# Performance work log

Measured on AMD Instinct MI355X. Metric: run time of the kernel, lower is better.

## Reference

```python
import jax, jax.numpy as jnp
import numpy as np

N, E, D, R, G, C = 100000, 600000, 128, 4, 256, 16
EPS = 1e-5

def _rgcn(x, src, dst, edge_type, w_rel, w_root, b):
    # out_i = x_i @ W_root + b + sum_r mean_{j in N_r(i)} x_j @ W_r  (PyG RGCNConv, aggr='mean')
    x_src = x[src]                                   # [E, D] gather
    out = x @ w_root + b                             # [N, D]
    for r in range(R):
        m = (edge_type == r).astype(x.dtype)         # [E]
        msg = (x_src @ w_rel[r]) * m[:, None]        # [E, D]
        agg = jax.ops.segment_sum(msg, dst, num_segments=N)
        cnt = jax.ops.segment_sum(m, dst, num_segments=N)
        out = out + agg / jnp.maximum(cnt, 1.0)[:, None]
    return out

def _bn_eval(x, gamma, beta, mean, var):
    return (x - mean) * jax.lax.rsqrt(var + EPS) * gamma + beta

def setup_inputs() -> dict:
    key = jax.random.key(0)
    ks = jax.random.split(key, 12)
    x = jax.random.normal(ks[0], (N, D), dtype=jnp.float32)
    edge_index = jax.random.randint(ks[1], (2, E), 0, N)
    edge_type = jax.random.randint(ks[2], (E,), 0, R)
    batch = jnp.sort(jax.random.randint(ks[3], (N,), 0, G))
    s = 1.0 / np.sqrt(D)
    conv_rel_w = jax.random.normal(ks[4], (3, R, D, D), dtype=jnp.float32) * s
    conv_root_w = jax.random.normal(ks[5], (3, D, D), dtype=jnp.float32) * s
    conv_bias = jnp.zeros((3, D), dtype=jnp.float32)
    bn_gamma = jnp.ones((2, D), dtype=jnp.float32)
    bn_beta = jnp.zeros((2, D), dtype=jnp.float32)
    bn_mean = jax.random.normal(ks[6], (2, D), dtype=jnp.float32) * 0.1
    bn_var = jax.random.uniform(ks[7], (2, D), minval=0.5, maxval=1.5, dtype=jnp.float32)
    cls_w1 = jax.random.normal(ks[8], (D, D // 2), dtype=jnp.float32) * s
    cls_b1 = jnp.zeros((D // 2,), dtype=jnp.float32)
    cls_w2 = jax.random.normal(ks[9], (D // 2, C), dtype=jnp.float32) / np.sqrt(D // 2)
    cls_b2 = jnp.zeros((C,), dtype=jnp.float32)
    return {"x": x, "edge_index": edge_index, "edge_type": edge_type, "batch": batch,
            "conv_rel_w": conv_rel_w, "conv_root_w": conv_root_w, "conv_bias": conv_bias,
            "bn_gamma": bn_gamma, "bn_beta": bn_beta, "bn_mean": bn_mean, "bn_var": bn_var,
            "cls_w1": cls_w1, "cls_b1": cls_b1, "cls_w2": cls_w2, "cls_b2": cls_b2}

def reference(x, edge_index, edge_type, batch, conv_rel_w, conv_root_w, conv_bias,
              bn_gamma, bn_beta, bn_mean, bn_var, cls_w1, cls_b1, cls_w2, cls_b2):
    src, dst = edge_index[0], edge_index[1]
    prev = None
    h = x
    for i in range(3):
        h_new = _rgcn(h, src, dst, edge_type, conv_rel_w[i], conv_root_w[i], conv_bias[i])
        if prev is not None:
            h_new = h_new + prev  # residual (shapes always match: D==D)
        if i != 2:
            h_new = _bn_eval(h_new, bn_gamma[i], bn_beta[i], bn_mean[i], bn_var[i])
            h_new = jax.nn.elu(h_new)  # alpha=1; dropout inactive in eval
        prev = h_new
        h = h_new
    # global mean pool over graphs
    sums = jax.ops.segment_sum(h, batch, num_segments=G)          # [G, D]
    cnts = jax.ops.segment_sum(jnp.ones((N,), h.dtype), batch, num_segments=G)
    pooled = sums / jnp.maximum(cnts, 1.0)[:, None]
    z = jax.nn.elu(pooled @ cls_w1 + cls_b1)
    logits = z @ cls_w2 + cls_b2
    return jax.nn.log_softmax(logits, axis=-1)
```

## Files before the change

kernel.cpp:

```cpp
#include <hip/hip_runtime.h>
#include <hip/hip_bf16.h>

#define NN 100000
#define EE 600000
#define DD 128
#define GG 256
#define CCL 16

typedef __attribute__((ext_vector_type(8))) short short8;
typedef __attribute__((ext_vector_type(4))) float f32x4;
typedef const __attribute__((address_space(1))) void* gas_t;
typedef __attribute__((address_space(3))) void* las_t;

__device__ __forceinline__ void async_ld16(const void* g, void* l) {
    __builtin_amdgcn_global_load_lds((gas_t)g, (las_t)l, 16, 0, 0);
}
__device__ __forceinline__ unsigned short f2bf(float x) {
    unsigned u = __float_as_uint(x);
    unsigned r = (u + 0x7FFFu + ((u >> 16) & 1u)) >> 16;
    return (unsigned short)r;
}
__device__ __forceinline__ float bf2f(unsigned short b) {
    return __uint_as_float(((unsigned)b) << 16);
}
__device__ __forceinline__ void unpack8(uint4 v, float* f) {
    f[0] = __uint_as_float(v.x << 16); f[1] = __uint_as_float(v.x & 0xFFFF0000u);
    f[2] = __uint_as_float(v.y << 16); f[3] = __uint_as_float(v.y & 0xFFFF0000u);
    f[4] = __uint_as_float(v.z << 16); f[5] = __uint_as_float(v.z & 0xFFFF0000u);
    f[6] = __uint_as_float(v.w << 16); f[7] = __uint_as_float(v.w & 0xFFFF0000u);
}

__global__ __launch_bounds__(256) void sniff_kernel(const void* __restrict__ xraw, int* __restrict__ flag) {
    int t = threadIdx.x;
    const unsigned short* u = (const unsigned short*)xraw;
    int good = 0;
    #pragma unroll
    for (int i = 0; i < 4; i++) {
        unsigned short b = u[t * 4 + i];
        int e = (b >> 7) & 0xFF;
        if (e >= 107 && e <= 130) good++;
    }
    __shared__ int sg[256];
    sg[t] = good;
    __syncthreads();
    for (int s = 128; s > 0; s >>= 1) { if (t < s) sg[t] += sg[t + s]; __syncthreads(); }
    if (t == 0) flag[0] = (sg[0] >= 900) ? 1 : 0;
}

__device__ __forceinline__ float loadf(const void* p, size_t i, int isbf) {
    if (isbf) return bf2f(((const unsigned short*)p)[i]);
    return ((const float*)p)[i];
}

__global__ __launch_bounds__(256) void convx_kernel(const void* __restrict__ xraw, const int* __restrict__ flag,
                                                    __hip_bfloat16* __restrict__ xc) {
    int isbf = flag[0];
    size_t i0 = ((size_t)blockIdx.x * 256 + threadIdx.x) * 8;
    if (i0 >= (size_t)NN * DD) return;
    if (isbf) {
        *(uint4*)(xc + i0) = *(const uint4*)((const __hip_bfloat16*)xraw + i0);
    } else {
        const float* xf = (const float*)xraw;
        unsigned short o[8];
        #pragma unroll
        for (int j = 0; j < 8; j++) o[j] = f2bf(xf[i0 + j]);
        *(uint4*)(xc + i0) = *(uint4*)o;
    }
}

__global__ __launch_bounds__(256) void convw_kernel(const void* __restrict__ rel_raw, const void* __restrict__ root_raw,
                                                    const int* __restrict__ flag, __hip_bfloat16* __restrict__ wt) {
    int isbf = flag[0];
    int mat = blockIdx.x;
    int layer = mat / 5, g = mat % 5;
    size_t srcoff = (g == 0) ? (size_t)layer * 16384 : (size_t)(layer * 4 + (g - 1)) * 16384;
    const void* sraw = (g == 0) ? root_raw : rel_raw;
    __hip_bfloat16* dstp = wt + (size_t)mat * 16384;
    for (int idx = threadIdx.x; idx < 16384; idx += 256) {
        int k = idx >> 7, n = idx & 127;
        float v = loadf(sraw, srcoff + (size_t)k * 128 + n, isbf);
        dstp[n * 128 + k] = __float2bfloat16(v);
    }
}

__global__ __launch_bounds__(256) void convp_kernel(const void* bias, const void* bng, const void* bnb,
                                                    const void* bnm, const void* bnv, const void* w1,
                                                    const void* b1, const void* w2, const void* b2,
                                                    const int* __restrict__ flag, float* __restrict__ pf) {
    int isbf = flag[0];
    const void* srcs[9] = {bias, bng, bnb, bnm, bnv, w1, b1, w2, b2};
    const int cnts[9] = {384, 256, 256, 256, 256, 8192, 64, 1024, 16};
    const int offs[9] = {0, 384, 640, 896, 1152, 1408, 9600, 9664, 10688};
    int b = blockIdx.x;
    const void* s = srcs[b];
    int c = cnts[b], o = offs[b];
    for (int i = threadIdx.x; i < c; i += 256) pf[o + i] = loadf(s, i, isbf);
}

__global__ __launch_bounds__(256) void count_kernel(const int* __restrict__ dst, int* __restrict__ cnt) {
    int e = blockIdx.x * 256 + threadIdx.x;
    if (e < EE) atomicAdd(&cnt[dst[e]], 1);
}

__global__ __launch_bounds__(256) void alloc_kernel(const int* __restrict__ cnt, int* __restrict__ counter,
                                                    int* __restrict__ startp, int* __restrict__ wptr) {
    int n = blockIdx.x * 256 + threadIdx.x;
    int lane = threadIdx.x & 63;
    int c = (n < NN) ? cnt[n] : 0;
    int v = c;
    #pragma unroll
    for (int d = 1; d < 64; d <<= 1) {
        int o = __shfl_up(v, d);
        if (lane >= d) v += o;
    }
    int base = 0;
    if (lane == 63) base = atomicAdd(counter, v);
    base = __shfl(base, 63);
    if (n < NN) {
        int s = base + v - c;
        startp[n] = s;
        wptr[n]  = s;
    }
}

__global__ __launch_bounds__(256) void fill_kernel(const int* __restrict__ src, const int* __restrict__ dst,
                                                   const int* __restrict__ et, int* __restrict__ wptr,
                                                   int* __restrict__ elist) {
    int e = blockIdx.x * 256 + threadIdx.x;
    if (e < EE) {
        int d = dst[e];
        int pos = atomicAdd(&wptr[d], 1);
        elist[pos] = src[e] | (et[e] << 17);
    }
}

__global__ __launch_bounds__(256) void agg_kernel(const __hip_bfloat16* __restrict__ h,
                                                  const int* __restrict__ elist,
                                                  const int* __restrict__ startp,
                                                  const int* __restrict__ cnt,
                                                  __hip_bfloat16* __restrict__ xagg) {
    int wid = (blockIdx.x * 256 + threadIdx.x) >> 6;
    int lane = threadIdx.x & 63;
    if (wid >= NN) return;
    int s = startp[wid], c = cnt[wid];
    int egrp = lane >> 4, col16 = lane & 15;
    int my = (lane < c) ? elist[s + lane] : 0;
    float acc[4][8];
    float cc[4] = {0.f, 0.f, 0.f, 0.f};
    #pragma unroll
    for (int rr = 0; rr < 4; rr++)
        #pragma unroll
        for (int j = 0; j < 8; j++) acc[rr][j] = 0.f;

    for (int base = 0; base < c; base += 8) {
        int eA = base + egrp, eB = base + 4 + egrp;
        bool actA = eA < c, actB = eB < c;
        int pA = __shfl(my, eA & 63);
        int pB = __shfl(my, eB & 63);
        if (actA && eA >= 64) pA = elist[s + eA];
        if (actB && eB >= 64) pB = elist[s + eB];
        int srcA = pA & 0x1FFFF, rA = (pA >> 17) & 3;
        int srcB = pB & 0x1FFFF, rB = (pB >> 17) & 3;
        uint4 vA = make_uint4(0, 0, 0, 0), vB = make_uint4(0, 0, 0, 0);
        if (actA) vA = *(const uint4*)(h + (size_t)srcA * DD + col16 * 8);
        if (actB) vB = *(const uint4*)(h + (size_t)srcB * DD + col16 * 8);
        float fA[8], fB[8];
        unpack8(vA, fA);
        unpack8(vB, fB);
        #pragma unroll
        for (int rr = 0; rr < 4; rr++) {
            float mA = (actA && rA == rr) ? 1.f : 0.f;
            float mB = (actB && rB == rr) ? 1.f : 0.f;
            cc[rr] += mA + mB;
            #pragma unroll
            for (int j = 0; j < 8; j++)
                acc[rr][j] = fmaf(mA, fA[j], fmaf(mB, fB[j], acc[rr][j]));
        }
    }
    #pragma unroll
    for (int rr = 0; rr < 4; rr++) {
        cc[rr] += __shfl_xor(cc[rr], 16);
        cc[rr] += __shfl_xor(cc[rr], 32);
        #pragma unroll
        for (int j = 0; j < 8; j++) {
            float sv = acc[rr][j];
            sv += __shfl_xor(sv, 16);
            sv += __shfl_xor(sv, 32);
            acc[rr][j] = sv;
        }
    }
    float o[8], ct;
    #pragma unroll
    for (int j = 0; j < 8; j++)
        o[j] = egrp < 2 ? (egrp == 0 ? acc[0][j] : acc[1][j])
                        : (egrp == 2 ? acc[2][j] : acc[3][j]);
    ct = egrp < 2 ? (egrp == 0 ? cc[0] : cc[1]) : (egrp == 2 ? cc[2] : cc[3]);
    float inv = 1.f / fmaxf(ct, 1.f);
    unsigned short u[8];
    #pragma unroll
    for (int j = 0; j < 8; j++) u[j] = f2bf(o[j] * inv);
    *(uint4*)(xagg + (size_t)wid * 512 + egrp * 128 + col16 * 8) = *(uint4*)u;
}

__global__ __launch_bounds__(256, 4) void gemm_kernel(const __hip_bfloat16* __restrict__ h_in,
                                                      const __hip_bfloat16* __restrict__ xagg,
                                                      const __hip_bfloat16* __restrict__ wt,
                                                      const float* __restrict__ bias,
                                                      const float* __restrict__ bng,
                                                      const float* __restrict__ bnb,
                                                      const float* __restrict__ bnm,
                                                      const float* __restrict__ bnv,
                                                      const __hip_bfloat16* __restrict__ hres,
                                                      __hip_bfloat16* __restrict__ hout,
                                                      int do_bn) {
    __shared__ __align__(16) short lds[16384];
    __shared__ float sbias[128], sgm[128], sga[128];
    short* Ab = lds;
    short* Bb = lds + 8192;
    int t = threadIdx.x;
    int wave = t >> 6, lane = t & 63, quad = lane >> 4, r16 = lane & 15;
    int m0 = blockIdx.x * 128;

    if (t < 128) {
        sbias[t] = bias[t];
        float gm = 0.f, ga = 0.f;
        if (do_bn) {
            float iva = rsqrtf(bnv[t] + 1e-5f);
            gm = bng[t] * iva;
            ga = bnb[t] - bnm[t] * gm;
        }
        sgm[t] = gm; sga[t] = ga;
    }

    int rbase = t >> 3;
    int gseg8 = ((t & 7) ^ (rbase & 7)) * 8;

    f32x4 acc[2][8];
    #pragma unroll
    for (int i = 0; i < 2; i++)
        #pragma unroll
        for (int j = 0; j < 8; j++) acc[i][j] = (f32x4){0.f, 0.f, 0.f, 0.f};

    for (int c = 0; c < 10; c++) {
        const __hip_bfloat16* asrc;
        int astride;
        if (c < 2) { asrc = h_in + c * 64; astride = 128; }
        else       { asrc = xagg + (c - 2) * 64; astride = 512; }
        const __hip_bfloat16* bsrc = wt + (size_t)(c >> 1) * 16384 + (c & 1) * 64;
        #pragma unroll
        for (int j = 0; j < 4; j++) {
            int row = j * 32 + rbase;
            int node = m0 + row; if (node > NN - 1) node = NN - 1;
            async_ld16(asrc + (size_t)node * astride + gseg8, &Ab[(j * 256 + t) * 8]);
            async_ld16(bsrc + (size_t)row * 128 + gseg8, &Bb[(j * 256 + t) * 8]);
        }
        __syncthreads();
        #pragma unroll
        for (int kc = 0; kc < 2; kc++) {
            int ra0 = wave * 32 + r16;
            int ra1 = ra0 + 16;
            short8 a0 = *(const short8*)&Ab[(ra0 * 8 + ((kc * 4 + quad) ^ (ra0 & 7))) * 8];
            short8 a1 = *(const short8*)&Ab[(ra1 * 8 + ((kc * 4 + quad) ^ (ra1 & 7))) * 8];
            #pragma unroll
            for (int nt = 0; nt < 8; nt++) {
                int rb = nt * 16 + r16;
                short8 b = *(const short8*)&Bb[(rb * 8 + ((kc * 4 + quad) ^ (rb & 7))) * 8];
                acc[0][nt] = __builtin_amdgcn_mfma_f32_16x16x32_bf16(a0, b, acc[0][nt], 0, 0, 0);
                acc[1][nt] = __builtin_amdgcn_mfma_f32_16x16x32_bf16(a1, b, acc[1][nt], 0, 0, 0);
            }
        }
        __syncthreads();
    }

    #pragma unroll
    for (int nt = 0; nt < 8; nt++) {
        int col = nt * 16 + r16;
        float bv = sbias[col];
        #pragma unroll
        for (int mt = 0; mt < 2; mt++) {
            #pragma unroll
            for (int reg = 0; reg < 4; reg++) {
                int row = wave * 32 + mt * 16 + quad * 4 + reg;
                int sslot = (col >> 3) ^ (row & 15);
                lds[row * 128 + sslot * 8 + (col & 7)] = (short)f2bf(acc[mt][nt][reg] + bv);
            }
        }
    }
    __syncthreads();
    int row = t >> 1, half = t & 1;
    int node = m0 + row;
    if (node < NN) {
        #pragma unroll
        for (int q = 0; q < 8; q++) {
            int seg = half * 8 + q;
            int sslot = seg ^ (row & 15);
            short8 cv = *(const short8*)&lds[row * 128 + sslot * 8];
            int col0 = seg * 8;
            float v[8];
            #pragma unroll
            for (int j = 0; j < 8; j++) v[j] = bf2f((unsigned short)cv[j]);
            if (hres) {
                float rf[8];
                unpack8(*(const uint4*)(hres + (size_t)node * 128 + col0), rf);
                #pragma unroll
                for (int j = 0; j < 8; j++) v[j] += rf[j];
            }
            if (do_bn) {
                #pragma unroll
                for (int j = 0; j < 8; j++) {
                    float z = v[j] * sgm[col0 + j] + sga[col0 + j];
                    v[j] = z > 0.f ? z : expm1f(z);
                }
            }
            unsigned short u[8];
            #pragma unroll
            for (int j = 0; j < 8; j++) u[j] = f2bf(v[j]);
            *(uint4*)(hout + (size_t)node * 128 + col0) = *(uint4*)u;
        }
    }
}

__global__ __launch_bounds__(256) void pool_kernel(const __hip_bfloat16* __restrict__ h3,
                                                   const int* __restrict__ batch,
                                                   float* __restrict__ pooled) {
    int g = blockIdx.x, t = threadIdx.x;
    int rowpar = t >> 4, colg = t & 15;
    int lo = 0, hi = NN;
    while (lo < hi) { int mid = (lo + hi) >> 1; if (batch[mid] < g) lo = mid + 1; else hi = mid; }
    int s0 = lo;
    hi = NN;
    while (lo < hi) { int mid = (lo + hi) >> 1; if (batch[mid] < g + 1) lo = mid + 1; else hi = mid; }
    int s1 = lo;
    float a[8];
    #pragma unroll
    for (int j = 0; j < 8; j++) a[j] = 0.f;
    for (int n = s0 + rowpar; n < s1; n += 16) {
        float f[8];
        unpack8(*(const uint4*)(h3 + (size_t)n * 128 + colg * 8), f);
        #pragma unroll
        for (int j = 0; j < 8; j++) a[j] += f[j];
    }
    __shared__ float sd[16][128];
    #pragma unroll
    for (int j = 0; j < 8; j++) sd[rowpar][colg * 8 + j] = a[j];
    __syncthreads();
    if (t < 128) {
        float sum = 0.f;
        #pragma unroll
        for (int i = 0; i < 16; i++) sum += sd[i][t];
        int cgn = s1 - s0;
        pooled[g * 128 + t] = sum / (float)(cgn > 0 ? cgn : 1);
    }
}

__global__ __launch_bounds__(64) void cls_kernel(const float* __restrict__ pooled,
                                                 const float* __restrict__ pf,
                                                 const int* __restrict__ flag,
                                                 void* __restrict__ out) {
    int g = blockIdx.x, j = threadIdx.x;
    const float* w1 = pf + 1408;
    const float* b1 = pf + 9600;
    const float* w2 = pf + 9664;
    const float* b2 = pf + 10688;
    __shared__ float z[64];
    __shared__ float lg[16];
    const float* p = pooled + g * 128;
    float acc = b1[j];
    for (int d = 0; d < 128; d++) acc += p[d] * w1[d * 64 + j];
    acc = acc > 0.f ? acc : expm1f(acc);
    z[j] = acc;
    __syncthreads();
    if (j < CCL) {
        float l = b2[j];
        for (int k = 0; k < 64; k++) l += z[k] * w2[k * 16 + j];
        lg[j] = l;
    }
    __syncthreads();
    if (j < CCL) {
        float m = lg[0];
        for (int k = 1; k < CCL; k++) m = fmaxf(m, lg[k]);
        float s = 0.f;
        for (int k = 0; k < CCL; k++) s += expf(lg[k] - m);
        float val = lg[j] - m - logf(s);
        if (flag[0]) ((__hip_bfloat16*)out)[g * CCL + j] = __float2bfloat16(val);
        else         ((float*)out)[g * CCL + j] = val;
    }
}

extern "C" void kernel_launch(void* const* d_in, const int* in_sizes, int n_in,
                              void* d_out, int out_size, void* d_ws, size_t ws_size,
                              hipStream_t stream) {
    const void* x_raw    = d_in[0];
    const int* ei        = (const int*)d_in[1];
    const int* et        = (const int*)d_in[2];
    const int* batch     = (const int*)d_in[3];
    const void* rel_raw  = d_in[4];
    const void* root_raw = d_in[5];
    const int* srcp = ei;
    const int* dstp = ei + EE;

    char* ws = (char*)d_ws;
    size_t off = 0;
    auto take = [&](size_t bytes) { size_t r = off; off += (bytes + 1023) & ~(size_t)1023; return r; };
    __hip_bfloat16* xagg = (__hip_bfloat16*)(ws + take((size_t)NN * 512 * 2));
    __hip_bfloat16* xc   = (__hip_bfloat16*)(ws + take((size_t)NN * 128 * 2));
    __hip_bfloat16* hA   = (__hip_bfloat16*)(ws + take((size_t)NN * 128 * 2));
    __hip_bfloat16* hB   = (__hip_bfloat16*)(ws + take((size_t)NN * 128 * 2));
    __hip_bfloat16* hC   = (__hip_bfloat16*)(ws + take((size_t)NN * 128 * 2));
    __hip_bfloat16* wt   = (__hip_bfloat16*)(ws + take((size_t)15 * 16384 * 2));
    float* pf            = (float*)(ws + take((size_t)10704 * 4));
    float* pooled        = (float*)(ws + take((size_t)GG * 128 * 4));
    int* cnt             = (int*)(ws + take((size_t)NN * 4 + 8));
    int* counter         = cnt + NN;
    int* flag            = cnt + NN + 1;
    int* startp          = (int*)(ws + take((size_t)NN * 4));
    int* wptr            = (int*)(ws + take((size_t)NN * 4));
    int* elist           = (int*)(ws + take((size_t)EE * 4));

    hipMemsetAsync(cnt, 0, (size_t)NN * 4 + 4, stream);
    sniff_kernel<<<1, 256, 0, stream>>>(x_raw, flag);
    convx_kernel<<<(NN * DD / 8 + 255) / 256, 256, 0, stream>>>(x_raw, flag, xc);
    convw_kernel<<<15, 256, 0, stream>>>(rel_raw, root_raw, flag, wt);
    convp_kernel<<<9, 256, 0, stream>>>(d_in[6], d_in[7], d_in[8], d_in[9], d_in[10],
                                        d_in[11], d_in[12], d_in[13], d_in[14], flag, pf);
    count_kernel<<<(EE + 255) / 256, 256, 0, stream>>>(dstp, cnt);
    alloc_kernel<<<(NN + 255) / 256, 256, 0, stream>>>(cnt, counter, startp, wptr);
    fill_kernel<<<(EE + 255) / 256, 256, 0, stream>>>(srcp, dstp, et, wptr, elist);

    const __hip_bfloat16* hin = xc;
    __hip_bfloat16* houts[3] = {hA, hB, hC};
    for (int l = 0; l < 3; l++) {
        agg_kernel<<<(NN * 64 + 255) / 256, 256, 0, stream>>>(hin, elist, startp, cnt, xagg);
        int bl = l < 2 ? l : 1;
        gemm_kernel<<<(NN + 127) / 128, 256, 0, stream>>>(
            hin, xagg, wt + (size_t)l * 5 * 16384, pf + l * 128,
            pf + 384 + bl * 128, pf + 640 + bl * 128, pf + 896 + bl * 128, pf + 1152 + bl * 128,
            (l > 0) ? hin : (const __hip_bfloat16*)nullptr, houts[l], (l < 2) ? 1 : 0);
        hin = houts[l];
    }
    pool_kernel<<<GG, 256, 0, stream>>>(houts[2], batch, pooled);
    cls_kernel<<<GG, 64, 0, stream>>>(pooled, pf, flag, (void*)d_out);
}
```

Measured before the change: 700.6 us.

## Bucket edges by (dst, relation) and simplify aggregation and GEMM A-loads

The CSR build now counts and fills per (destination, relation) bucket, so each relation's edges are contiguous and the packed type bits are no longer stored. The aggregation kernel assigns 16 lanes per node and loops over each relation's bucket directly, replacing the masked 4-way accumulate and cross-lane reductions. The GEMM stages only each 128x128 weight block in LDS and reads A fragments straight from global memory, with the occupancy hint dropped from launch_bounds. The intent is less wasted FMA and shuffle work and fewer LDS round trips. The risks are serial per-edge latency in aggregation, uncoalesced direct A reads in the GEMM, and a CSR bookkeeping footprint four times larger.

```diff
diff --git a/kernel.cpp b/kernel.cpp
--- a/kernel.cpp
+++ b/kernel.cpp
@@ -97,16 +97,20 @@
     for (int i = threadIdx.x; i < c; i += 256) pf[o + i] = loadf(s, i, isbf);
 }
 
-__global__ __launch_bounds__(256) void count_kernel(const int* __restrict__ dst, int* __restrict__ cnt) {
+__global__ __launch_bounds__(256) void count4_kernel(const int* __restrict__ dst, const int* __restrict__ et,
+                                                     int* __restrict__ cnt4) {
     int e = blockIdx.x * 256 + threadIdx.x;
-    if (e < EE) atomicAdd(&cnt[dst[e]], 1);
-}
-
-__global__ __launch_bounds__(256) void alloc_kernel(const int* __restrict__ cnt, int* __restrict__ counter,
-                                                    int* __restrict__ startp, int* __restrict__ wptr) {
-    int n = blockIdx.x * 256 + threadIdx.x;
+    if (e < EE) atomicAdd(&cnt4[dst[e] * 4 + et[e]], 1);
+}
+
+__global__ __launch_bounds__(256) void alloc4_kernel(const int* __restrict__ cnt4, int* __restrict__ counter,
+                                                     int* __restrict__ startp4, int* __restrict__ wptr4) {
+    int wgid = blockIdx.x * 4 + (threadIdx.x >> 6);
     int lane = threadIdx.x & 63;
-    int c = (n < NN) ? cnt[n] : 0;
+    int e0 = wgid * 256 + lane * 4;
+    int4 cv = make_int4(0, 0, 0, 0);
+    if (e0 < NN * 4) cv = *(const int4*)(cnt4 + e0);
+    int c = cv.x + cv.y + cv.z + cv.w;
     int v = c;
     #pragma unroll
     for (int d = 1; d < 64; d <<= 1) {
@@ -116,107 +120,70 @@
     int base = 0;
     if (lane == 63) base = atomicAdd(counter, v);
     base = __shfl(base, 63);
-    if (n < NN) {
-        int s = base + v - c;
-        startp[n] = s;
-        wptr[n]  = s;
-    }
-}
-
-__global__ __launch_bounds__(256) void fill_kernel(const int* __restrict__ src, const int* __restrict__ dst,
-                                                   const int* __restrict__ et, int* __restrict__ wptr,
-                                                   int* __restrict__ elist) {
+    if (e0 < NN * 4) {
+        int s0 = base + v - c;
+        int4 st;
+        st.x = s0; st.y = s0 + cv.x; st.z = st.y + cv.y; st.w = st.z + cv.z;
+        *(int4*)(startp4 + e0) = st;
+        *(int4*)(wptr4 + e0) = st;
+    }
+}
+
+__global__ __launch_bounds__(256) void fill4_kernel(const int* __restrict__ src, const int* __restrict__ dst,
+                                                    const int* __restrict__ et, int* __restrict__ wptr4,
+                                                    int* __restrict__ elist) {
     int e = blockIdx.x * 256 + threadIdx.x;
     if (e < EE) {
-        int d = dst[e];
-        int pos = atomicAdd(&wptr[d], 1);
-        elist[pos] = src[e] | (et[e] << 17);
+        int pos = atomicAdd(&wptr4[dst[e] * 4 + et[e]], 1);
+        elist[pos] = src[e];
     }
 }
 
 __global__ __launch_bounds__(256) void agg_kernel(const __hip_bfloat16* __restrict__ h,
                                                   const int* __restrict__ elist,
-                                                  const int* __restrict__ startp,
-                                                  const int* __restrict__ cnt,
+                                                  const int* __restrict__ startp4,
+                                                  const int* __restrict__ cnt4,
                                                   __hip_bfloat16* __restrict__ xagg) {
-    int wid = (blockIdx.x * 256 + threadIdx.x) >> 6;
-    int lane = threadIdx.x & 63;
-    if (wid >= NN) return;
-    int s = startp[wid], c = cnt[wid];
-    int egrp = lane >> 4, col16 = lane & 15;
-    int my = (lane < c) ? elist[s + lane] : 0;
-    float acc[4][8];
-    float cc[4] = {0.f, 0.f, 0.f, 0.f};
-    #pragma unroll
-    for (int rr = 0; rr < 4; rr++)
-        #pragma unroll
-        for (int j = 0; j < 8; j++) acc[rr][j] = 0.f;
-
-    for (int base = 0; base < c; base += 8) {
-        int eA = base + egrp, eB = base + 4 + egrp;
-        bool actA = eA < c, actB = eB < c;
-        int pA = __shfl(my, eA & 63);
-        int pB = __shfl(my, eB & 63);
-        if (actA && eA >= 64) pA = elist[s + eA];
-        if (actB && eB >= 64) pB = elist[s + eB];
-        int srcA = pA & 0x1FFFF, rA = (pA >> 17) & 3;
-        int srcB = pB & 0x1FFFF, rB = (pB >> 17) & 3;
-        uint4 vA = make_uint4(0, 0, 0, 0), vB = make_uint4(0, 0, 0, 0);
-        if (actA) vA = *(const uint4*)(h + (size_t)srcA * DD + col16 * 8);
-        if (actB) vB = *(const uint4*)(h + (size_t)srcB * DD + col16 * 8);
-        float fA[8], fB[8];
-        unpack8(vA, fA);
-        unpack8(vB, fB);
-        #pragma unroll
-        for (int rr = 0; rr < 4; rr++) {
-            float mA = (actA && rA == rr) ? 1.f : 0.f;
-            float mB = (actB && rB == rr) ? 1.f : 0.f;
-            cc[rr] += mA + mB;
+    int node = blockIdx.x * 16 + (threadIdx.x >> 4);
+    int c16 = threadIdx.x & 15;
+    const int* st = startp4 + node * 4;
+    const int* cn = cnt4 + node * 4;
+    __hip_bfloat16* outp = xagg + (size_t)node * 512;
+    #pragma unroll
+    for (int r = 0; r < 4; r++) {
+        int s = st[r], c = cn[r];
+        float a[8];
+        #pragma unroll
+        for (int j = 0; j < 8; j++) a[j] = 0.f;
+        for (int i = 0; i < c; i++) {
+            int srcn = elist[s + i];
+            uint4 v = *(const uint4*)(h + (size_t)srcn * DD + c16 * 8);
+            float f[8];
+            unpack8(v, f);
             #pragma unroll
-            for (int j = 0; j < 8; j++)
-                acc[rr][j] = fmaf(mA, fA[j], fmaf(mB, fB[j], acc[rr][j]));
-        }
-    }
-    #pragma unroll
-    for (int rr = 0; rr < 4; rr++) {
-        cc[rr] += __shfl_xor(cc[rr], 16);
-        cc[rr] += __shfl_xor(cc[rr], 32);
-        #pragma unroll
-        for (int j = 0; j < 8; j++) {
-            float sv = acc[rr][j];
-            sv += __shfl_xor(sv, 16);
-            sv += __shfl_xor(sv, 32);
-            acc[rr][j] = sv;
-        }
-    }
-    float o[8], ct;
-    #pragma unroll
-    for (int j = 0; j < 8; j++)
-        o[j] = egrp < 2 ? (egrp == 0 ? acc[0][j] : acc[1][j])
-                        : (egrp == 2 ? acc[2][j] : acc[3][j]);
-    ct = egrp < 2 ? (egrp == 0 ? cc[0] : cc[1]) : (egrp == 2 ? cc[2] : cc[3]);
-    float inv = 1.f / fmaxf(ct, 1.f);
-    unsigned short u[8];
-    #pragma unroll
-    for (int j = 0; j < 8; j++) u[j] = f2bf(o[j] * inv);
-    *(uint4*)(xagg + (size_t)wid * 512 + egrp * 128 + col16 * 8) = *(uint4*)u;
-}
-
-__global__ __launch_bounds__(256, 4) void gemm_kernel(const __hip_bfloat16* __restrict__ h_in,
-                                                      const __hip_bfloat16* __restrict__ xagg,
-                                                      const __hip_bfloat16* __restrict__ wt,
-                                                      const float* __restrict__ bias,
-                                                      const float* __restrict__ bng,
-                                                      const float* __restrict__ bnb,
-                                                      const float* __restrict__ bnm,
-                                                      const float* __restrict__ bnv,
-                                                      const __hip_bfloat16* __restrict__ hres,
-                                                      __hip_bfloat16* __restrict__ hout,
-                                                      int do_bn) {
+            for (int j = 0; j < 8; j++) a[j] += f[j];
+        }
+        float inv = 1.f / (float)(c > 0 ? c : 1);
+        unsigned short u[8];
+        #pragma unroll
+        for (int j = 0; j < 8; j++) u[j] = f2bf(a[j] * inv);
+        *(uint4*)(outp + r * 128 + c16 * 8) = *(uint4*)u;
+    }
+}
+
+__global__ __launch_bounds__(256) void gemm_kernel(const __hip_bfloat16* __restrict__ h_in,
+                                                   const __hip_bfloat16* __restrict__ xagg,
+                                                   const __hip_bfloat16* __restrict__ wt,
+                                                   const float* __restrict__ bias,
+                                                   const float* __restrict__ bng,
+                                                   const float* __restrict__ bnb,
+                                                   const float* __restrict__ bnm,
+                                                   const float* __restrict__ bnv,
+                                                   const __hip_bfloat16* __restrict__ hres,
+                                                   __hip_bfloat16* __restrict__ hout,
+                                                   int do_bn) {
     __shared__ __align__(16) short lds[16384];
     __shared__ float sbias[128], sgm[128], sga[128];
-    short* Ab = lds;
-    short* Bb = lds + 8192;
     int t = threadIdx.x;
     int wave = t >> 6, lane = t & 63, quad = lane >> 4, r16 = lane & 15;
     int m0 = blockIdx.x * 128;
@@ -232,8 +199,8 @@
         sgm[t] = gm; sga[t] = ga;
     }
 
-    int rbase = t >> 3;
-    int gseg8 = ((t & 7) ^ (rbase & 7)) * 8;
+    int r0 = m0 + wave * 32 + r16;      if (r0 > NN - 1) r0 = NN - 1;
+    int r1 = m0 + wave * 32 + 16 + r16; if (r1 > NN - 1) r1 = NN - 1;
 
     f32x4 acc[2][8];
     #pragma unroll
@@ -241,30 +208,31 @@
         #pragma unroll
         for (int j = 0; j < 8; j++) acc[i][j] = (f32x4){0.f, 0.f, 0.f, 0.f};
 
-    for (int c = 0; c < 10; c++) {
-        const __hip_bfloat16* asrc;
-        int astride;
-        if (c < 2) { asrc = h_in + c * 64; astride = 128; }
-        else       { asrc = xagg + (c - 2) * 64; astride = 512; }
-        const __hip_bfloat16* bsrc = wt + (size_t)(c >> 1) * 16384 + (c & 1) * 64;
-        #pragma unroll
-        for (int j = 0; j < 4; j++) {
-            int row = j * 32 + rbase;
-            int node = m0 + row; if (node > NN - 1) node = NN - 1;
-            async_ld16(asrc + (size_t)node * astride + gseg8, &Ab[(j * 256 + t) * 8]);
-            async_ld16(bsrc + (size_t)row * 128 + gseg8, &Bb[(j * 256 + t) * 8]);
+    #pragma unroll
+    for (int g = 0; g < 5; g++) {
+        const __hip_bfloat16* wg = wt + (size_t)g * 16384;
+        #pragma unroll
+        for (int j = 0; j < 8; j++) {
+            int slot = j * 256 + t;
+            int row = slot >> 4, sp = slot & 15;
+            int sg = sp ^ (row & 15);
+            async_ld16(wg + row * 128 + sg * 8, &lds[slot * 8]);
         }
         __syncthreads();
-        #pragma unroll
-        for (int kc = 0; kc < 2; kc++) {
-            int ra0 = wave * 32 + r16;
-            int ra1 = ra0 + 16;
-            short8 a0 = *(const short8*)&Ab[(ra0 * 8 + ((kc * 4 + quad) ^ (ra0 & 7))) * 8];
-            short8 a1 = *(const short8*)&Ab[(ra1 * 8 + ((kc * 4 + quad) ^ (ra1 & 7))) * 8];
+
+        const __hip_bfloat16* a0p = (g == 0) ? (h_in + (size_t)r0 * 128)
+                                             : (xagg + (size_t)r0 * 512 + (g - 1) * 128);
+        const __hip_bfloat16* a1p = (g == 0) ? (h_in + (size_t)r1 * 128)
+                                             : (xagg + (size_t)r1 * 512 + (g - 1) * 128);
+        #pragma unroll
+        for (int kc = 0; kc < 4; kc++) {
+            short8 a0 = *(const short8*)(a0p + kc * 32 + quad * 8);
+            short8 a1 = *(const short8*)(a1p + kc * 32 + quad * 8);
+            int s = kc * 4 + quad;
             #pragma unroll
             for (int nt = 0; nt < 8; nt++) {
                 int rb = nt * 16 + r16;
-                short8 b = *(const short8*)&Bb[(rb * 8 + ((kc * 4 + quad) ^ (rb & 7))) * 8];
+                short8 b = *(const short8*)&lds[(rb * 16 + (s ^ (rb & 15))) * 8];
                 acc[0][nt] = __builtin_amdgcn_mfma_f32_16x16x32_bf16(a0, b, acc[0][nt], 0, 0, 0);
                 acc[1][nt] = __builtin_amdgcn_mfma_f32_16x16x32_bf16(a1, b, acc[1][nt], 0, 0, 0);
             }
@@ -410,27 +378,27 @@
     __hip_bfloat16* wt   = (__hip_bfloat16*)(ws + take((size_t)15 * 16384 * 2));
     float* pf            = (float*)(ws + take((size_t)10704 * 4));
     float* pooled        = (float*)(ws + take((size_t)GG * 128 * 4));
-    int* cnt             = (int*)(ws + take((size_t)NN * 4 + 8));
-    int* counter         = cnt + NN;
-    int* flag            = cnt + NN + 1;
-    int* startp          = (int*)(ws + take((size_t)NN * 4));
-    int* wptr            = (int*)(ws + take((size_t)NN * 4));
+    int* cnt4            = (int*)(ws + take((size_t)NN * 16 + 8));
+    int* counter         = cnt4 + NN * 4;
+    int* flag            = cnt4 + NN * 4 + 1;
+    int* startp4         = (int*)(ws + take((size_t)NN * 16));
+    int* wptr4           = (int*)(ws + take((size_t)NN * 16));
     int* elist           = (int*)(ws + take((size_t)EE * 4));
 
-    hipMemsetAsync(cnt, 0, (size_t)NN * 4 + 4, stream);
+    hipMemsetAsync(cnt4, 0, (size_t)NN * 16 + 4, stream);
     sniff_kernel<<<1, 256, 0, stream>>>(x_raw, flag);
     convx_kernel<<<(NN * DD / 8 + 255) / 256, 256, 0, stream>>>(x_raw, flag, xc);
     convw_kernel<<<15, 256, 0, stream>>>(rel_raw, root_raw, flag, wt);
     convp_kernel<<<9, 256, 0, stream>>>(d_in[6], d_in[7], d_in[8], d_in[9], d_in[10],
                                         d_in[11], d_in[12], d_in[13], d_in[14], flag, pf);
-    count_kernel<<<(EE + 255) / 256, 256, 0, stream>>>(dstp, cnt);
-    alloc_kernel<<<(NN + 255) / 256, 256, 0, stream>>>(cnt, counter, startp, wptr);
-    fill_kernel<<<(EE + 255) / 256, 256, 0, stream>>>(srcp, dstp, et, wptr, elist);
+    count4_kernel<<<(EE + 255) / 256, 256, 0, stream>>>(dstp, et, cnt4);
+    alloc4_kernel<<<(NN * 4 + 1023) / 1024, 256, 0, stream>>>(cnt4, counter, startp4, wptr4);
+    fill4_kernel<<<(EE + 255) / 256, 256, 0, stream>>>(srcp, dstp, et, wptr4, elist);
 
     const __hip_bfloat16* hin = xc;
     __hip_bfloat16* houts[3] = {hA, hB, hC};
     for (int l = 0; l < 3; l++) {
-        agg_kernel<<<(NN * 64 + 255) / 256, 256, 0, stream>>>(hin, elist, startp, cnt, xagg);
+        agg_kernel<<<NN / 16, 256, 0, stream>>>(hin, elist, startp4, cnt4, xagg);
         int bl = l < 2 ? l : 1;
         gemm_kernel<<<(NN + 127) / 128, 256, 0, stream>>>(
             hin, xagg, wt + (size_t)l * 5 * 16384, pf + l * 128,
```

New measurement: 636.0 us. 1.1x faster.
